# Performance work log

Hardware: AMD Instinct MI355X
Metric: run time of the kernel (lower is better)

## Reference

```python
import jax, jax.numpy as jnp
import numpy as np
import math

EMBED = 1024
HEADS = 16
HEAD_DIM = EMBED // HEADS


def setup_inputs() -> dict:
    key = jax.random.key(0)
    ks = jax.random.split(key, 9)
    B, S = 2, 2048
    query = jax.random.normal(ks[0], (B, S, EMBED), dtype=jnp.float32)
    key_t = jax.random.normal(ks[1], (B, S, EMBED), dtype=jnp.float32)
    value = jax.random.normal(ks[2], (B, S, EMBED), dtype=jnp.float32)
    mask = jax.random.randint(ks[3], (B, 1, S, S), 0, 2, dtype=jnp.int32)
    # nn.Linear(head_dim, head_dim, bias=False) weights: [out, in]
    sc = 1.0 / math.sqrt(HEAD_DIM)
    Wq = jax.random.uniform(ks[4], (HEAD_DIM, HEAD_DIM), jnp.float32, -sc, sc)
    Wk = jax.random.uniform(ks[5], (HEAD_DIM, HEAD_DIM), jnp.float32, -sc, sc)
    Wv = jax.random.uniform(ks[6], (HEAD_DIM, HEAD_DIM), jnp.float32, -sc, sc)
    so = 1.0 / math.sqrt(EMBED)
    Wo = jax.random.uniform(ks[7], (EMBED, EMBED), jnp.float32, -so, so)
    bo = jax.random.uniform(ks[8], (EMBED,), jnp.float32, -so, so)
    return {"query": query, "key": key_t, "value": value, "mask": mask,
            "Wq": Wq, "Wk": Wk, "Wv": Wv, "Wo": Wo, "bo": bo}


def reference(query, key, value, mask, Wq, Wk, Wv, Wo, bo):
    B, Sq, E = query.shape
    Sk = key.shape[1]
    H, D = HEADS, HEAD_DIM
    # Faithful raw reshape into heads (as in the torch source, no transpose)
    q = query.reshape(B, H, Sq, D)
    k = key.reshape(B, H, Sk, D)
    v = value.reshape(B, H, Sk, D)
    # per-head_dim Linear (bias-free): x @ W.T
    Q = jnp.einsum('bhsd,ed->bhse', q, Wq)
    K = jnp.einsum('bhsd,ed->bhse', k, Wk)
    V = jnp.einsum('bhsd,ed->bhse', v, Wv)
    scores = jnp.einsum('bhqd,bhkd->bhqk', Q, K)  # [B,H,Sq,Sk]
    scores = jnp.where(mask == 0, jnp.float32(-1e20), scores)
    # NOTE: source divides by sqrt(embed_size), not sqrt(head_dim)
    attn = jax.nn.softmax(scores / jnp.float32(math.sqrt(E)), axis=-1)
    out = jnp.einsum('bhqk,bhkd->bhqd', attn, V).reshape(B, Sq, H * D)
    return out @ Wo.T + bo
```

## Files before the change

### kernel.cpp

```cpp
#include <hip/hip_runtime.h>

typedef __attribute__((ext_vector_type(8))) short short8;
typedef __attribute__((ext_vector_type(4))) float f32x4;
typedef __attribute__((ext_vector_type(2))) int int2v;
typedef __attribute__((ext_vector_type(4))) int int4v;

__device__ __forceinline__ short f2bf(float f) {
  unsigned u = __builtin_bit_cast(unsigned, f);
  u += 0x7fff + ((u >> 16) & 1);
  return (short)(u >> 16);
}

__device__ __forceinline__ int pk2bf(float lo, float hi) {
#if defined(__gfx950__) && __has_builtin(__builtin_amdgcn_cvt_pk_bf16_f32)
  typedef __attribute__((ext_vector_type(2))) __bf16 bf16x2;
  bf16x2 v = __builtin_amdgcn_cvt_pk_bf16_f32(lo, hi);
  return __builtin_bit_cast(int, v);
#else
  return (int)(unsigned short)(short)f2bf(lo) | (((int)f2bf(hi)) << 16);
#endif
}

__device__ __forceinline__ int pktr(float lo, float hi) {
  return (int)(__builtin_bit_cast(unsigned, lo) >> 16) |
         (int)(__builtin_bit_cast(unsigned, hi) & 0xffff0000u);
}

__device__ __forceinline__ short8 pack8(f32x4 a, f32x4 b) {
  int4v t;
  t.x = pk2bf(a[0], a[1]);
  t.y = pk2bf(a[2], a[3]);
  t.z = pk2bf(b[0], b[1]);
  t.w = pk2bf(b[2], b[3]);
  return __builtin_bit_cast(short8, t);
}

__device__ __forceinline__ float fand(float p, int m) {
  return __builtin_bit_cast(float, __builtin_bit_cast(int, p) & m);
}

__device__ __forceinline__ int bmask(unsigned w, int bit) {
#if __has_builtin(__builtin_amdgcn_sbfe)
  return __builtin_amdgcn_sbfe((int)w, bit, 1);
#else
  return ((int)(w << (31 - bit))) >> 31;
#endif
}

__device__ __forceinline__ float fexp2(float x) {
#if __has_builtin(__builtin_amdgcn_exp2f)
  return __builtin_amdgcn_exp2f(x);
#else
  return exp2f(x);
#endif
}

__device__ __forceinline__ void glds16(const short* g, short* lbase, int lane) {
#if __has_builtin(__builtin_amdgcn_global_load_lds)
  __builtin_amdgcn_global_load_lds(
      (const __attribute__((address_space(1))) unsigned int*)g,
      (__attribute__((address_space(3))) unsigned int*)lbase, 16, 0, 0);
#else
  *(short8*)(lbase + lane * 8) = *(const short8*)g;
#endif
}

__global__ __launch_bounds__(256) void prep(const float* __restrict__ q,
                                            const float* __restrict__ k,
                                            const float* __restrict__ v,
                                            const float* __restrict__ Wq,
                                            const float* __restrict__ Wk,
                                            const float* __restrict__ Wv,
                                            const float* __restrict__ Wo,
                                            const int* __restrict__ mask,
                                            short* __restrict__ Qp,
                                            short* __restrict__ Kp,
                                            short* __restrict__ Vtp,
                                            short* __restrict__ Wob,
                                            unsigned* __restrict__ mmod) {
  const int bid = blockIdx.x;
  const int tid = threadIdx.x;

  if (bid >= 4096) {
    const int mb = bid - 4096;
    const int kp = mb & 15, bq = mb >> 4;
    const int b_ = bq >> 5, q64 = bq & 31;
    const int wv = tid >> 6, qd = (tid >> 4) & 3, m16_ = tid & 15;
    unsigned d = 0;
#pragma unroll
    for (int hb = 0; hb < 2; ++hb) {
      const int* mr = mask + b_ * 4194304 + (q64 * 64 + wv * 16 + m16_) * 2048 +
                      (kp * 2 + hb) * 64 + qd * 4;
#pragma unroll
      for (int grp = 0; grp < 4; ++grp)
#pragma unroll
        for (int r = 0; r < 4; ++r)
          if (mr[grp * 16 + r] != 0) d |= 1u << (hb * 16 + grp * 4 + r);
    }
    mmod[mb * 256 + tid] = d;
    return;
  }
  if (bid >= 3072) {
    const int i = ((bid - 3072) * 256 + tid) * 4;
    const f32x4 x = *(const f32x4*)&Wo[i];
    int2v o;
    o.x = pk2bf(x[0], x[1]);
    o.y = pk2bf(x[2], x[3]);
    *(int2v*)&Wob[i] = o;
    return;
  }

  __shared__ short xt[64][72];
  __shared__ short ot[64][72];
  const int mode = bid >> 10;
  const int bt = bid & 1023;
  const float* X;
  const float* W;
  float scale;
  if (mode == 0) { X = q; W = Wq; scale = 0.045084220f; }
  else if (mode == 1) { X = k; W = Wk; scale = 1.0f; }
  else { X = v; W = Wv; scale = 1.0f; }

  const int r0 = bt * 64;
  const int row = tid >> 2, seg = (tid & 3) * 16;
  const f32x4* xs = (const f32x4*)(X + (r0 + row) * 64 + seg);
  const f32x4 x0 = xs[0], x1 = xs[1], x2 = xs[2], x3 = xs[3];
  *(short8*)&xt[row][seg] = pack8(x0, x1);
  *(short8*)&xt[row][seg + 8] = pack8(x2, x3);
  __syncthreads();

  const int lane = tid & 63, wave = tid >> 6;
  const int m16 = lane & 15, quad = lane >> 4;

  const short8 a0 = *(const short8*)&xt[wave * 16 + m16][quad * 8];
  const short8 a1 = *(const short8*)&xt[wave * 16 + m16][32 + quad * 8];

  f32x4 acc[4];
#pragma unroll
  for (int nt = 0; nt < 4; ++nt) {
    const f32x4* wp0 = (const f32x4*)&W[(nt * 16 + m16) * 64 + quad * 8];
    const f32x4* wp1 = (const f32x4*)&W[(nt * 16 + m16) * 64 + 32 + quad * 8];
    const short8 b0 = pack8(wp0[0], wp0[1]);
    const short8 b1 = pack8(wp1[0], wp1[1]);
    f32x4 z = (f32x4){0.f, 0.f, 0.f, 0.f};
    z = __builtin_amdgcn_mfma_f32_16x16x32_bf16(a0, b0, z, 0, 0, 0);
    z = __builtin_amdgcn_mfma_f32_16x16x32_bf16(a1, b1, z, 0, 0, 0);
    acc[nt] = z;
  }

  if (mode != 2) {
#pragma unroll
    for (int nt = 0; nt < 4; ++nt)
#pragma unroll
      for (int r = 0; r < 4; ++r)
        ot[wave * 16 + quad * 4 + r][nt * 16 + m16] = f2bf(acc[nt][r] * scale);
  } else {
#pragma unroll
    for (int nt = 0; nt < 4; ++nt)
#pragma unroll
      for (int r = 0; r < 4; ++r)
        ot[nt * 16 + m16][quad * 8 + (wave & 1) * 4 + r + (wave >> 1) * 32] =
            f2bf(acc[nt][r]);
  }
  __syncthreads();

  const int orow = tid >> 2, opart = tid & 3;
  if (mode != 2) {
    short* dst = (mode == 0 ? Qp : Kp) + (r0 + orow) * 64 + opart * 16;
    *(short8*)&dst[0] = *(const short8*)&ot[orow][opart * 16];
    *(short8*)&dst[8] = *(const short8*)&ot[orow][opart * 16 + 8];
  } else {
    const int bh = r0 >> 11, s0 = r0 & 2047;
    short* dst = Vtp + bh * 131072 + orow * 2048 + s0 + opart * 16;
    *(short8*)&dst[0] = *(const short8*)&ot[orow][opart * 16];
    *(short8*)&dst[8] = *(const short8*)&ot[orow][opart * 16 + 8];
  }
}

__global__ __launch_bounds__(256) void flash64r(const short* __restrict__ Qp,
                                                const short* __restrict__ Kp,
                                                const short* __restrict__ Vt,
                                                const unsigned* __restrict__ mmod,
                                                short* __restrict__ Ob) {
  __shared__ __attribute__((aligned(16))) short kt0[4096];
  __shared__ __attribute__((aligned(16))) short kt1[4096];
  __shared__ __attribute__((aligned(16))) short vt0[4096];
  __shared__ __attribute__((aligned(16))) short vt1[4096];
  __shared__ __attribute__((aligned(16))) short pt[4096];
  const int tid = threadIdx.x;
  const int bid = blockIdx.x;
  const int local = bid >> 3;
  const int qblk = local & 31;
  const int bh = (bid & 7) * 4 + (local >> 5);
  const int q0 = qblk << 6;
  const int b = bh >> 4;
  const short* Qh = Qp + bh * 131072;
  const short* Kh = Kp + bh * 131072;
  const short* Vh = Vt + bh * 131072;
  const int lane = tid & 63, wave = tid >> 6;
  const int m16 = lane & 15, quad = lane >> 4;
  const int srow = lane >> 3, sj = (lane & 7) ^ srow;
  const int koff = m16 * 128 + ((quad ^ (m16 & 7)) * 16);
  const unsigned* mq = mmod + ((b * 32 + qblk) * 16) * 256 + wave * 64 + quad * 16 + m16;

  char* const ptB = (char*)pt;

  short8 aq[2];
#pragma unroll
  for (int h = 0; h < 2; ++h)
    aq[h] = *(const short8*)&Qh[(q0 + wave * 16 + m16) * 64 + h * 32 + quad * 8];

  float l = 0.f;
  f32x4 oacc[4];
#pragma unroll
  for (int dt = 0; dt < 4; ++dt) oacc[dt] = (f32x4){0.f, 0.f, 0.f, 0.f};

  auto stage = [&](short* ktb, short* vtb, int ka) {
#pragma unroll
    for (int t = 0; t < 2; ++t) {
      const int crow = wave * 16 + t * 8;
      glds16(Kh + (ka * 64 + crow + srow) * 64 + sj * 8, ktb + crow * 64, lane);
      glds16(Vh + (crow + srow) * 2048 + ka * 64 + sj * 8, vtb + crow * 64, lane);
    }
  };

  auto compute = [&](const short* ktp, const short* vtp, unsigned mw, int bb) {
    const char* ktb = (const char*)ktp;
    const char* vtb = (const char*)vtp;
    f32x4 s[4];
    __builtin_amdgcn_s_setprio(1);
#pragma unroll
    for (int grp = 0; grp < 4; ++grp) {
      const int o0 = grp * 2048 + koff;
      const short8 kb0 = *(const short8*)(ktb + o0);
      const short8 kb1 = *(const short8*)(ktb + (o0 ^ 64));
      f32x4 z = (f32x4){0.f, 0.f, 0.f, 0.f};
      z = __builtin_amdgcn_mfma_f32_16x16x32_bf16(kb0, aq[0], z, 0, 0, 0);
      z = __builtin_amdgcn_mfma_f32_16x16x32_bf16(kb1, aq[1], z, 0, 0, 0);
      s[grp] = z;
    }
    __builtin_amdgcn_s_setprio(0);

    float p[4][4];
#pragma unroll
    for (int grp = 0; grp < 4; ++grp)
#pragma unroll
      for (int r = 0; r < 4; ++r)
        p[grp][r] = fand(fexp2(s[grp][r]), bmask(mw, bb + grp * 4 + r));
    float g0 = (p[0][0] + p[0][1]) + (p[0][2] + p[0][3]);
    float g1 = (p[1][0] + p[1][1]) + (p[1][2] + p[1][3]);
    float g2 = (p[2][0] + p[2][1]) + (p[2][2] + p[2][3]);
    float g3 = (p[3][0] + p[3][1]) + (p[3][2] + p[3][3]);
    l += (g0 + g1) + (g2 + g3);

    int4v t0, t1;
    t0.x = pktr(p[0][0], p[0][1]);
    t0.y = pktr(p[0][2], p[0][3]);
    t0.z = pktr(p[1][0], p[1][1]);
    t0.w = pktr(p[1][2], p[1][3]);
    t1.x = pktr(p[2][0], p[2][1]);
    t1.y = pktr(p[2][2], p[2][3]);
    t1.z = pktr(p[3][0], p[3][1]);
    t1.w = pktr(p[3][2], p[3][3]);
    const short8 ap0 = __builtin_bit_cast(short8, t0);
    const short8 ap1 = __builtin_bit_cast(short8, t1);

    __builtin_amdgcn_s_setprio(1);
#pragma unroll
    for (int dt = 0; dt < 4; ++dt) {
      const int o0 = dt * 2048 + koff;
      const short8 vb0 = *(const short8*)(vtb + o0);
      const short8 vb1 = *(const short8*)(vtb + (o0 ^ 64));
      f32x4 z = oacc[dt];
      z = __builtin_amdgcn_mfma_f32_16x16x32_bf16(ap0, vb0, z, 0, 0, 0);
      z = __builtin_amdgcn_mfma_f32_16x16x32_bf16(ap1, vb1, z, 0, 0, 0);
      oacc[dt] = z;
    }
    __builtin_amdgcn_s_setprio(0);
  };

  unsigned mw = mq[0];
  stage(kt0, vt0, 0);
  stage(kt1, vt1, 1);

  for (int kk = 0; kk < 15; ++kk) {
    const unsigned mwn = mq[(kk + 1) * 256];
    asm volatile("s_waitcnt vmcnt(5)" ::: "memory");
    __builtin_amdgcn_s_barrier();
    compute(kt0, vt0, mw, 0);
    __builtin_amdgcn_s_barrier();
    stage(kt0, vt0, 2 * kk + 2);
    asm volatile("s_waitcnt vmcnt(5)" ::: "memory");
    __builtin_amdgcn_s_barrier();
    compute(kt1, vt1, mw, 16);
    __builtin_amdgcn_s_barrier();
    stage(kt1, vt1, 2 * kk + 3);
    mw = mwn;
  }
  asm volatile("s_waitcnt vmcnt(4)" ::: "memory");
  __builtin_amdgcn_s_barrier();
  compute(kt0, vt0, mw, 0);
  asm volatile("s_waitcnt vmcnt(0)" ::: "memory");
  __builtin_amdgcn_s_barrier();
  compute(kt1, vt1, mw, 16);

  l += __shfl_xor(l, 16);
  l += __shfl_xor(l, 32);
  float linv[4];
#pragma unroll
  for (int r = 0; r < 4; ++r) linv[r] = 1.0f / __shfl(l, quad * 4 + r, 64);

#pragma unroll
  for (int r = 0; r < 4; ++r) {
    const int row = wave * 16 + quad * 4 + r;
#pragma unroll
    for (int dt = 0; dt < 4; ++dt)
      *(short*)(ptB + row * 128 + ((dt * 32 + m16 * 2) ^ ((row & 7) << 4))) =
          f2bf(oacc[dt][r] * linv[r]);
  }
  asm volatile("s_waitcnt lgkmcnt(0)" ::: "memory");

  const int orow = lane >> 2, opart = lane & 3;
  const int prow = wave * 16 + orow;
  const int oswz = (orow & 7) << 4;
  short* og = Ob + (bh * 2048 + q0 + prow) * 64 + opart * 16;
  *(short8*)&og[0] = *(const short8*)(ptB + prow * 128 + ((opart * 32) ^ oswz));
  *(short8*)&og[8] = *(const short8*)(ptB + prow * 128 + ((opart * 32 + 16) ^ oswz));
}

__global__ __launch_bounds__(256) void outproj(const short* __restrict__ Ob,
                                               const short* __restrict__ Wob,
                                               const float* __restrict__ bo,
                                               float* __restrict__ out) {
  __shared__ short at[64][72];
  __shared__ short bt[128][72];
  const int tid = threadIdx.x;
  const int bid = blockIdx.x;
  const int ct = bid >> 6, rt = bid & 63;
  const int r0 = rt * 64, c0 = ct * 128;
  const int lane = tid & 63, wave = tid >> 6;
  const int mr = (wave >> 1) * 32, nc = (wave & 1) * 64;
  const int m16 = lane & 15, quad = lane >> 4;
  const int arow = tid >> 2, apart = tid & 3;
  const int brow = tid >> 1, bhalf = (tid & 1) * 32;

  f32x4 acc[2][4];
#pragma unroll
  for (int mt = 0; mt < 2; ++mt)
#pragma unroll
    for (int nt = 0; nt < 4; ++nt) acc[mt][nt] = (f32x4){0.f, 0.f, 0.f, 0.f};

  for (int kc = 0; kc < 16; ++kc) {
    __syncthreads();
    const short* ag = &Ob[(r0 + arow) * 1024 + kc * 64 + apart * 16];
    const short* bg = &Wob[(c0 + brow) * 1024 + kc * 64 + bhalf];
    *(short8*)&at[arow][apart * 16] = *(const short8*)&ag[0];
    *(short8*)&at[arow][apart * 16 + 8] = *(const short8*)&ag[8];
    *(short8*)&bt[brow][bhalf] = *(const short8*)&bg[0];
    *(short8*)&bt[brow][bhalf + 8] = *(const short8*)&bg[8];
    *(short8*)&bt[brow][bhalf + 16] = *(const short8*)&bg[16];
    *(short8*)&bt[brow][bhalf + 24] = *(const short8*)&bg[24];
    __syncthreads();

#pragma unroll
    for (int kh = 0; kh < 2; ++kh) {
      short8 af[2], bf[4];
#pragma unroll
      for (int i = 0; i < 2; ++i)
        af[i] = *(const short8*)&at[mr + i * 16 + m16][kh * 32 + quad * 8];
#pragma unroll
      for (int j = 0; j < 4; ++j)
        bf[j] = *(const short8*)&bt[nc + j * 16 + m16][kh * 32 + quad * 8];
#pragma unroll
      for (int mt = 0; mt < 2; ++mt)
#pragma unroll
        for (int nt = 0; nt < 4; ++nt)
          acc[mt][nt] = __builtin_amdgcn_mfma_f32_16x16x32_bf16(af[mt], bf[nt], acc[mt][nt], 0, 0, 0);
    }
  }

#pragma unroll
  for (int nt = 0; nt < 4; ++nt) {
    const int col = c0 + nc + nt * 16 + m16;
    const float bias = bo[col];
#pragma unroll
    for (int mt = 0; mt < 2; ++mt)
#pragma unroll
      for (int rr2 = 0; rr2 < 4; ++rr2)
        out[(r0 + mr + mt * 16 + quad * 4 + rr2) * 1024 + col] = acc[mt][nt][rr2] + bias;
  }
}

extern "C" void kernel_launch(void* const* d_in, const int* in_sizes, int n_in,
                              void* d_out, int out_size, void* d_ws, size_t ws_size,
                              hipStream_t stream) {
  const float* query = (const float*)d_in[0];
  const float* key = (const float*)d_in[1];
  const float* value = (const float*)d_in[2];
  const int* mask = (const int*)d_in[3];
  const float* Wq = (const float*)d_in[4];
  const float* Wk = (const float*)d_in[5];
  const float* Wv = (const float*)d_in[6];
  const float* Wo = (const float*)d_in[7];
  const float* bo = (const float*)d_in[8];
  float* out = (float*)d_out;

  char* ws = (char*)d_ws;
  short* Qp = (short*)(ws);
  short* Kp = (short*)(ws + 8388608);
  short* Vt = (short*)(ws + 16777216);
  short* Ob = (short*)(ws + 25165824);
  short* Wob = (short*)(ws + 41943040);
  unsigned* mmod = (unsigned*)(ws + 44564480);

  prep<<<5120, 256, 0, stream>>>(query, key, value, Wq, Wk, Wv, Wo, mask,
                                 Qp, Kp, Vt, Wob, mmod);
  flash64r<<<1024, 256, 0, stream>>>(Qp, Kp, Vt, mmod, Ob);
  outproj<<<512, 256, 0, stream>>>(Ob, Wob, bo, out);
}
```

Before: 220.2 us.

## Compute softmax row sums via MFMA, reuse LDS, double-buffer outproj loads

In the flash kernel, the scalar per-lane row-sum accumulation and cross-lane shuffles are replaced by an extra pair of MFMAs against a ones vector. The dedicated output staging buffer is dropped by reusing the K tile buffer, which shrinks LDS use. The output projection moves from synchronous register-staged LDS loads to double-buffered direct global-to-LDS loads with an XOR swizzle and waitcnt-based pipelining. The extra MFMAs add matrix work but remove VALU adds, and the sums now come from bf16-rounded probabilities, which slightly changes numerics.

```diff
diff --git a/kernel.cpp b/kernel.cpp
--- a/kernel.cpp
+++ b/kernel.cpp
@@ -186,7 +186,6 @@
   __shared__ __attribute__((aligned(16))) short kt1[4096];
   __shared__ __attribute__((aligned(16))) short vt0[4096];
   __shared__ __attribute__((aligned(16))) short vt1[4096];
-  __shared__ __attribute__((aligned(16))) short pt[4096];
   const int tid = threadIdx.x;
   const int bid = blockIdx.x;
   const int local = bid >> 3;
@@ -203,14 +202,15 @@
   const int koff = m16 * 128 + ((quad ^ (m16 & 7)) * 16);
   const unsigned* mq = mmod + ((b * 32 + qblk) * 16) * 256 + wave * 64 + quad * 16 + m16;
 
-  char* const ptB = (char*)pt;
+  const short onebf = (short)0x3F80;
+  const short8 ones = (short8){onebf, onebf, onebf, onebf, onebf, onebf, onebf, onebf};
 
   short8 aq[2];
 #pragma unroll
   for (int h = 0; h < 2; ++h)
     aq[h] = *(const short8*)&Qh[(q0 + wave * 16 + m16) * 64 + h * 32 + quad * 8];
 
-  float l = 0.f;
+  f32x4 oaccL = (f32x4){0.f, 0.f, 0.f, 0.f};
   f32x4 oacc[4];
 #pragma unroll
   for (int dt = 0; dt < 4; ++dt) oacc[dt] = (f32x4){0.f, 0.f, 0.f, 0.f};
@@ -247,11 +247,6 @@
 #pragma unroll
       for (int r = 0; r < 4; ++r)
         p[grp][r] = fand(fexp2(s[grp][r]), bmask(mw, bb + grp * 4 + r));
-    float g0 = (p[0][0] + p[0][1]) + (p[0][2] + p[0][3]);
-    float g1 = (p[1][0] + p[1][1]) + (p[1][2] + p[1][3]);
-    float g2 = (p[2][0] + p[2][1]) + (p[2][2] + p[2][3]);
-    float g3 = (p[3][0] + p[3][1]) + (p[3][2] + p[3][3]);
-    l += (g0 + g1) + (g2 + g3);
 
     int4v t0, t1;
     t0.x = pktr(p[0][0], p[0][1]);
@@ -266,6 +261,8 @@
     const short8 ap1 = __builtin_bit_cast(short8, t1);
 
     __builtin_amdgcn_s_setprio(1);
+    oaccL = __builtin_amdgcn_mfma_f32_16x16x32_bf16(ap0, ones, oaccL, 0, 0, 0);
+    oaccL = __builtin_amdgcn_mfma_f32_16x16x32_bf16(ap1, ones, oaccL, 0, 0, 0);
 #pragma unroll
     for (int dt = 0; dt < 4; ++dt) {
       const int o0 = dt * 2048 + koff;
@@ -304,12 +301,11 @@
   __builtin_amdgcn_s_barrier();
   compute(kt1, vt1, mw, 16);
 
-  l += __shfl_xor(l, 16);
-  l += __shfl_xor(l, 32);
   float linv[4];
 #pragma unroll
-  for (int r = 0; r < 4; ++r) linv[r] = 1.0f / __shfl(l, quad * 4 + r, 64);
-
+  for (int r = 0; r < 4; ++r) linv[r] = 1.0f / oaccL[r];
+
+  char* const ptB = (char*)kt0;
 #pragma unroll
   for (int r = 0; r < 4; ++r) {
     const int row = wave * 16 + quad * 4 + r;
@@ -332,8 +328,10 @@
                                                const short* __restrict__ Wob,
                                                const float* __restrict__ bo,
                                                float* __restrict__ out) {
-  __shared__ short at[64][72];
-  __shared__ short bt[128][72];
+  __shared__ __attribute__((aligned(16))) short at0[4096];
+  __shared__ __attribute__((aligned(16))) short at1[4096];
+  __shared__ __attribute__((aligned(16))) short bt0[8192];
+  __shared__ __attribute__((aligned(16))) short bt1[8192];
   const int tid = threadIdx.x;
   const int bid = blockIdx.x;
   const int ct = bid >> 6, rt = bid & 63;
@@ -341,8 +339,8 @@
   const int lane = tid & 63, wave = tid >> 6;
   const int mr = (wave >> 1) * 32, nc = (wave & 1) * 64;
   const int m16 = lane & 15, quad = lane >> 4;
-  const int arow = tid >> 2, apart = tid & 3;
-  const int brow = tid >> 1, bhalf = (tid & 1) * 32;
+  const int srow = lane >> 3, sj = (lane & 7) ^ srow;
+  const int mswz = (m16 & 7) << 4;
 
   f32x4 acc[2][4];
 #pragma unroll
@@ -350,34 +348,61 @@
 #pragma unroll
     for (int nt = 0; nt < 4; ++nt) acc[mt][nt] = (f32x4){0.f, 0.f, 0.f, 0.f};
 
-  for (int kc = 0; kc < 16; ++kc) {
-    __syncthreads();
-    const short* ag = &Ob[(r0 + arow) * 1024 + kc * 64 + apart * 16];
-    const short* bg = &Wob[(c0 + brow) * 1024 + kc * 64 + bhalf];
-    *(short8*)&at[arow][apart * 16] = *(const short8*)&ag[0];
-    *(short8*)&at[arow][apart * 16 + 8] = *(const short8*)&ag[8];
-    *(short8*)&bt[brow][bhalf] = *(const short8*)&bg[0];
-    *(short8*)&bt[brow][bhalf + 8] = *(const short8*)&bg[8];
-    *(short8*)&bt[brow][bhalf + 16] = *(const short8*)&bg[16];
-    *(short8*)&bt[brow][bhalf + 24] = *(const short8*)&bg[24];
-    __syncthreads();
-
+  auto stageK = [&](short* atb, short* btb, int kc) {
+#pragma unroll
+    for (int t = 0; t < 2; ++t) {
+      const int crow = wave * 16 + t * 8;
+      glds16(Ob + (r0 + crow + srow) * 1024 + kc * 64 + sj * 8, atb + crow * 64, lane);
+    }
+#pragma unroll
+    for (int t = 0; t < 4; ++t) {
+      const int crow = wave * 32 + t * 8;
+      glds16(Wob + (c0 + crow + srow) * 1024 + kc * 64 + sj * 8, btb + crow * 64, lane);
+    }
+  };
+
+  auto computeK = [&](const short* atp, const short* btp) {
+    const char* atB = (const char*)atp;
+    const char* btB = (const char*)btp;
 #pragma unroll
     for (int kh = 0; kh < 2; ++kh) {
       short8 af[2], bf[4];
 #pragma unroll
       for (int i = 0; i < 2; ++i)
-        af[i] = *(const short8*)&at[mr + i * 16 + m16][kh * 32 + quad * 8];
+        af[i] = *(const short8*)(atB + (mr + i * 16 + m16) * 128 +
+                                 ((kh * 64 + quad * 16) ^ mswz));
 #pragma unroll
       for (int j = 0; j < 4; ++j)
-        bf[j] = *(const short8*)&bt[nc + j * 16 + m16][kh * 32 + quad * 8];
+        bf[j] = *(const short8*)(btB + (nc + j * 16 + m16) * 128 +
+                                 ((kh * 64 + quad * 16) ^ mswz));
+      __builtin_amdgcn_s_setprio(1);
 #pragma unroll
       for (int mt = 0; mt < 2; ++mt)
 #pragma unroll
         for (int nt = 0; nt < 4; ++nt)
-          acc[mt][nt] = __builtin_amdgcn_mfma_f32_16x16x32_bf16(af[mt], bf[nt], acc[mt][nt], 0, 0, 0);
-    }
-  }
+          acc[mt][nt] = __builtin_amdgcn_mfma_f32_16x16x32_bf16(af[mt], bf[nt],
+                                                                acc[mt][nt], 0, 0, 0);
+      __builtin_amdgcn_s_setprio(0);
+    }
+  };
+
+  stageK(at0, bt0, 0);
+  stageK(at1, bt1, 1);
+  for (int kc = 0; kc < 14; ++kc) {
+    short* atb = (kc & 1) ? at1 : at0;
+    short* btb = (kc & 1) ? bt1 : bt0;
+    asm volatile("s_waitcnt vmcnt(6)" ::: "memory");
+    __builtin_amdgcn_s_barrier();
+    computeK(atb, btb);
+    __builtin_amdgcn_s_barrier();
+    stageK(atb, btb, kc + 2);
+  }
+  asm volatile("s_waitcnt vmcnt(6)" ::: "memory");
+  __builtin_amdgcn_s_barrier();
+  computeK(at0, bt0);
+  asm volatile("s_waitcnt vmcnt(0)" ::: "memory");
+  __builtin_amdgcn_s_barrier();
+  computeK(at1, bt1);
 
 #pragma unroll
   for (int nt = 0; nt < 4; ++nt) {
```

After: 218.4 us. Within noise of the previous version (-0.8%).
